# Optimization experiments

Measured on AMD Instinct MI355X. Metric: run time of the kernel, lower is better.

The kernel has to match this reference:

```python
import jax, jax.numpy as jnp
import numpy as np

H, K, D, HID, B = 8, 2048, 64, 1024, 8192
TEMP = 1.0
LN_EPS = 1e-5


def setup_inputs() -> dict:
    key = jax.random.key(0)
    ks = jax.random.split(key, 6)
    s = lambda k, shape, scale=0.02: jax.random.normal(k, shape, jnp.float32) * scale
    return dict(
        z=jax.random.normal(ks[0], (B, HID), jnp.float32),
        w1=s(ks[1], (H, HID, 2 * D)),
        b1=jnp.zeros((H, 2 * D), jnp.float32),
        w2=s(ks[2], (H, 2 * D, D)),
        b2=jnp.zeros((H, D), jnp.float32),
        ln_g=jnp.ones((H, D), jnp.float32),
        ln_b=jnp.zeros((H, D), jnp.float32),
        codebooks=jax.random.normal(ks[3], (H, K, D), jnp.float32) * 0.1,
        dec_w=s(ks[4], (H, D, HID // H)),
        dec_b=jnp.zeros((H, HID // H), jnp.float32),
    )


def reference(z, w1, b1, w2, b2, ln_g, ln_b, codebooks, dec_w, dec_b):
    sg = jax.lax.stop_gradient
    Bf = z.shape[0]
    # per-head projection MLP (all heads fused via einsum): [B,HID] -> [B,H,2D] -> [B,H,D]
    h1 = jax.nn.gelu(jnp.einsum('bi,hio->bho', z, w1) + b1, approximate=False)
    zh = jnp.einsum('bho,hod->bhd', h1, w2) + b2
    mu = zh.mean(-1, keepdims=True)
    var = zh.var(-1, keepdims=True)  # biased, as torch LayerNorm
    z_heads = (zh - mu) / jnp.sqrt(var + LN_EPS) * ln_g + ln_b  # [B,H,D]
    # squared-distance to codebooks: ||z||^2 + ||c||^2 - 2 z.c  -> [B,H,K]
    z_sq = (z_heads ** 2).sum(-1)[..., None]          # [B,H,1]
    c_sq = (codebooks ** 2).sum(-1)[None]             # [1,H,K]
    zc = jnp.einsum('bhd,hkd->bhk', z_heads, codebooks)
    dists = z_sq + c_sq - 2.0 * zc
    idx = jnp.argmin(dists, axis=-1)                  # [B,H] int
    z_q = codebooks[jnp.arange(H)[None, :], idx]      # gather -> [B,H,D]
    # per-head decoders then concat -> [B,HID]
    dec = lambda x: (jnp.einsum('bhd,hdo->bho', x, dec_w) + dec_b).reshape(Bf, -1)
    z_q_dec = dec(z_q)
    z_proj = dec(z_heads)
    z_q_st = z_proj + sg(z_q_dec - z_proj)
    commit = jnp.mean((z_proj - sg(z_q_dec)) ** 2)
    codebook_loss = jnp.mean((sg(z_proj) - z_q_dec) ** 2)
    # entropy regularizer over soft assignment probs
    probs = jax.nn.softmax(-dists * TEMP, axis=-1)    # [B,H,K]
    avg_probs = probs.mean(0)                         # [H,K]
    entropy = -(avg_probs * jnp.log(avg_probs + 1e-8)).sum(-1).mean()
    entropy_loss = 1.0 - entropy / np.float32(np.log(K))
    # orthogonality: pairwise co-occurrence deviation from independence
    p = jnp.zeros((H, K), jnp.float32).at[jnp.arange(H)[None, :], idx].add(1.0) / Bf  # [H,K]
    ortho = jnp.float32(0.0)
    cnt = 0
    for i in range(H):
        for j in range(i + 1, H):
            co = jnp.zeros((K, K), jnp.float32).at[idx[:, i], idx[:, j]].add(1.0) / (Bf + 1e-8)
            expected = p[i][:, None] * p[j][None, :]
            ortho = ortho + jnp.mean(jnp.abs(co - expected))
            cnt += 1
    ortho = ortho / cnt
    return z_q_st, idx, commit, codebook_loss, entropy_loss, ortho, sg(z_heads)
```

## Files before the change

kernel.cpp:

```cpp
#include <hip/hip_runtime.h>
#include <math.h>

#define H 8
#define KK 2048
#define DD 64
#define HIDN 1024
#define BB 8192
#define TWO_D 128
#define OO 128

#define WS_CSQ   1048576
#define WS_ZSQ   1064960
#define WS_IDX   1130496
#define WS_AVGP  1196032
#define WS_HIST  1212416
#define WS_ACC   1228800
#define WS_ZERO_BYTES ((16384 + 16384 + 4) * 4)

#define OUT_ZQ 0
#define OUT_IDX 8388608
#define OUT_COMMIT 8454144
#define OUT_CBL 8454145
#define OUT_ENT 8454146
#define OUT_ORTHO 8454147
#define OUT_ZH 8454148
#define W2P_OFF 3145728

typedef __attribute__((ext_vector_type(8))) short bf16x8;
typedef __attribute__((ext_vector_type(4))) float f32x4;

__device__ inline unsigned short bf16_rne(float x) {
    union { float f; unsigned u; } c; c.f = x;
    unsigned r = c.u + 0x7FFFu + ((c.u >> 16) & 1u);
    return (unsigned short)(r >> 16);
}
__device__ inline float bf16_f32(unsigned short h) {
    union { unsigned u; float f; } c; c.u = ((unsigned)h) << 16;
    return c.f;
}
__device__ inline void split3(float x, short* hh, short* mm, short* ll) {
    unsigned short h_ = bf16_rne(x);
    float r1 = x - bf16_f32(h_);
    unsigned short m_ = bf16_rne(r1);
    float r2 = r1 - bf16_f32(m_);
    unsigned short l_ = bf16_rne(r2);
    *hh = (short)h_; *mm = (short)m_; *ll = (short)l_;
}

__device__ inline void gload_lds16(const void* g, void* l) {
    __builtin_amdgcn_global_load_lds(
        (const __attribute__((address_space(1))) unsigned int*)g,
        (__attribute__((address_space(3))) unsigned int*)l, 16, 0, 0);
}

__global__ __launch_bounds__(256) void k_pre_w1(const float* __restrict__ w1, float* outp) {
    short* w1p = (short*)outp;
    int h = blockIdx.x >> 5, kc = blockIdx.x & 31;
    int t = threadIdx.x;
    int l = t & 63, w = t >> 6;
    int lb = l & 15, lg = l >> 4;
#pragma unroll
    for (int oi = 0; oi < 2; ++oi) {
        int ot = w + oi * 4;
        union { short e[8]; bf16x8 v; } uh, um, ul;
#pragma unroll
        for (int j = 0; j < 8; ++j) {
            float x = w1[(size_t)(h * HIDN + kc * 32 + lg * 8 + j) * TWO_D + ot * 16 + lb];
            split3(x, &uh.e[j], &um.e[j], &ul.e[j]);
        }
        size_t base = (((size_t)(h * 32 + kc) * 8 + ot) * 3) * 512 + l * 8;
        *(bf16x8*)(w1p + base) = uh.v;
        *(bf16x8*)(w1p + base + 512) = um.v;
        *(bf16x8*)(w1p + base + 1024) = ul.v;
    }
}

__global__ __launch_bounds__(256) void k_pre_w2(const float* __restrict__ w2, float* outp) {
    short* w2p = (short*)outp + W2P_OFF;
    int h = blockIdx.x;
    int t = threadIdx.x;
    int l = t & 63, w = t >> 6;
    int lb = l & 15, lg = l >> 4;
#pragma unroll
    for (int i = 0; i < 4; ++i) {
        int fr = w * 4 + i;
        int dt = fr >> 2, oc = fr & 3;
        union { short e[8]; bf16x8 v; } uh, um, ul;
#pragma unroll
        for (int j = 0; j < 8; ++j) {
            float x = w2[(size_t)(h * TWO_D + oc * 32 + lg * 8 + j) * DD + dt * 16 + lb];
            split3(x, &uh.e[j], &um.e[j], &ul.e[j]);
        }
        size_t base = (((size_t)(h * 4 + dt) * 4 + oc) * 3) * 512 + l * 8;
        *(bf16x8*)(w2p + base) = uh.v;
        *(bf16x8*)(w2p + base + 512) = um.v;
        *(bf16x8*)(w2p + base + 1024) = ul.v;
    }
}

__global__ __launch_bounds__(256) void k_pre(const float* __restrict__ cb, float* __restrict__ ws) {
    int h = blockIdx.x >> 3, kb = blockIdx.x & 7;
    int t = threadIdx.x;
    int lb = t & 15, lg = (t >> 4) & 3;
    short* stg = (short*)ws;
#pragma unroll
    for (int p = 0; p < 4; ++p) {
        int tloc = p * 4 + (t >> 6);
        int T = kb * 16 + tloc;
        int k = T * 16 + lb;
        const float* row = cb + (size_t)(h * KK + k) * DD;
        float4 a0 = *(const float4*)(row + lg * 8);
        float4 a1 = *(const float4*)(row + lg * 8 + 4);
        float4 c0 = *(const float4*)(row + 32 + lg * 8);
        float4 c1 = *(const float4*)(row + 32 + lg * 8 + 4);
        float v0[8] = {a0.x, a0.y, a0.z, a0.w, a1.x, a1.y, a1.z, a1.w};
        float v1[8] = {c0.x, c0.y, c0.z, c0.w, c1.x, c1.y, c1.z, c1.w};
        union { short e[8]; bf16x8 v; } h0, h1, l0, l1;
        float s = 0.f;
#pragma unroll
        for (int j = 0; j < 8; ++j) {
            float x = v0[j];
            s = fmaf(x, x, s);
            unsigned short hb = bf16_rne(x);
            h0.e[j] = (short)hb;
            l0.e[j] = (short)bf16_rne(x - bf16_f32(hb));
            float y = v1[j];
            s = fmaf(y, y, s);
            unsigned short hb2 = bf16_rne(y);
            h1.e[j] = (short)hb2;
            l1.e[j] = (short)bf16_rne(y - bf16_f32(hb2));
        }
        size_t base = (((size_t)(h * 128 + T) * 4) * 64 + (t & 63)) * 8;
        *(bf16x8*)(stg + base) = h0.v;
        *(bf16x8*)(stg + base + 512) = h1.v;
        *(bf16x8*)(stg + base + 1024) = l0.v;
        *(bf16x8*)(stg + base + 1536) = l1.v;
        s += __shfl_xor(s, 16);
        s += __shfl_xor(s, 32);
        if (lg == 0) ws[WS_CSQ + h * KK + k] = s;
    }
}

__global__ __launch_bounds__(512, 4) void k1(const float* __restrict__ z, const float* __restrict__ b1,
                                             const float* __restrict__ b2, const float* __restrict__ lng,
                                             const float* __restrict__ lnb, float* out,
                                             float* __restrict__ ws) {
    __shared__ char SM[51200];
    int t = threadIdx.x;
    int h = blockIdx.y;
    int b0 = blockIdx.x * 64;
    int w = t >> 6, l = t & 63;
    int rg = w >> 1, wc = w & 1;
    int lb = l & 15, lg = l >> 4;

    const short* w2p = (const short*)out + W2P_OFF;
    const char* w1h = (const char*)out + (size_t)h * (32 * 24576);
    const float* zrow = z + (size_t)(b0 + rg * 16 + lb) * HIDN + lg * 8;

    {
        char* lb0 = SM + (t >> 6) * 1024;
        const char* gb = w1h + t * 16;
#pragma unroll
        for (int r = 0; r < 3; ++r) gload_lds16(gb + r * 8192, lb0 + r * 8192);
#pragma unroll
        for (int r = 0; r < 3; ++r) gload_lds16(gb + 24576 + r * 8192, lb0 + 24576 + r * 8192);
    }
    float4 zA = *(const float4*)(zrow);
    float4 zB = *(const float4*)(zrow + 4);
    __syncthreads();

    f32x4 acc[4];
#pragma unroll
    for (int i = 0; i < 4; ++i) acc[i] = (f32x4){0.f, 0.f, 0.f, 0.f};

#pragma unroll
    for (int c = 0; c < 32; ++c) {
        if (c > 0) {
            if (c < 31) asm volatile("s_waitcnt vmcnt(3)" ::: "memory");
            else        asm volatile("s_waitcnt vmcnt(0)" ::: "memory");
            __builtin_amdgcn_sched_barrier(0);
            __builtin_amdgcn_s_barrier();
            __builtin_amdgcn_sched_barrier(0);
        }
        {
            float zc[8] = {zA.x, zA.y, zA.z, zA.w, zB.x, zB.y, zB.z, zB.w};
            union { short e[8]; bf16x8 v; } uh, um, ul;
#pragma unroll
            for (int j = 0; j < 8; ++j) split3(zc[j], &uh.e[j], &um.e[j], &ul.e[j]);
            bf16x8 bh = uh.v, bm = um.v, blo = ul.v;
            const char* bp = SM + (c & 1) * 24576;
#pragma unroll
            for (int ot = 0; ot < 4; ++ot) {
                const char* fb = bp + (wc * 4 + ot) * 3072 + l * 16;
                bf16x8 ah = *(const bf16x8*)(fb);
                bf16x8 am = *(const bf16x8*)(fb + 1024);
                bf16x8 al = *(const bf16x8*)(fb + 2048);
                f32x4 cc = acc[ot];
                cc = __builtin_amdgcn_mfma_f32_16x16x32_bf16(ah, bh, cc, 0, 0, 0);
                cc = __builtin_amdgcn_mfma_f32_16x16x32_bf16(ah, bm, cc, 0, 0, 0);
                cc = __builtin_amdgcn_mfma_f32_16x16x32_bf16(am, bh, cc, 0, 0, 0);
                cc = __builtin_amdgcn_mfma_f32_16x16x32_bf16(ah, blo, cc, 0, 0, 0);
                cc = __builtin_amdgcn_mfma_f32_16x16x32_bf16(al, bh, cc, 0, 0, 0);
                cc = __builtin_amdgcn_mfma_f32_16x16x32_bf16(am, bm, cc, 0, 0, 0);
                acc[ot] = cc;
            }
        }
        __builtin_amdgcn_sched_barrier(0);
        __builtin_amdgcn_s_barrier();
        __builtin_amdgcn_sched_barrier(0);
        if (c < 31) {
            zA = *(const float4*)(zrow + (c + 1) * 32);
            zB = *(const float4*)(zrow + (c + 1) * 32 + 4);
        }
        if (c + 2 < 32) {
            char* lb0 = SM + (c & 1) * 24576 + (t >> 6) * 1024;
            const char* gb = w1h + (size_t)(c + 2) * 24576 + t * 16;
#pragma unroll
            for (int r = 0; r < 3; ++r) gload_lds16(gb + r * 8192, lb0 + r * 8192);
        }
    }
    __syncthreads();

    float* h1L = (float*)SM;
    float* zhL = (float*)(SM + 33792);

#pragma unroll
    for (int ot = 0; ot < 4; ++ot)
#pragma unroll
        for (int r = 0; r < 4; ++r) {
            int o = (wc * 4 + ot) * 16 + lg * 4 + r;
            float x = acc[ot][r] + b1[h * TWO_D + o];
            float gl = 0.5f * x * (1.0f + erff(x * 0.70710678118654752f));
            h1L[(rg * 16 + lb) * 132 + o] = gl;
        }
    __syncthreads();

    f32x4 a2[2];
    a2[0] = (f32x4){0.f, 0.f, 0.f, 0.f};
    a2[1] = (f32x4){0.f, 0.f, 0.f, 0.f};
#pragma unroll
    for (int oc = 0; oc < 4; ++oc) {
        const float* hr = h1L + (rg * 16 + lb) * 132 + oc * 32 + lg * 8;
        union { short e[8]; bf16x8 v; } uh, um, ul;
#pragma unroll
        for (int j = 0; j < 8; ++j) split3(hr[j], &uh.e[j], &um.e[j], &ul.e[j]);
        bf16x8 bh = uh.v, bm = um.v, blo = ul.v;
#pragma unroll
        for (int dti = 0; dti < 2; ++dti) {
            int dt = wc * 2 + dti;
            const short* fb = w2p + (((size_t)(h * 4 + dt) * 4 + oc) * 3) * 512 + l * 8;
            bf16x8 ah = *(const bf16x8*)(fb);
            bf16x8 am = *(const bf16x8*)(fb + 512);
            bf16x8 al = *(const bf16x8*)(fb + 1024);
            f32x4 cc = a2[dti];
            cc = __builtin_amdgcn_mfma_f32_16x16x32_bf16(ah, bh, cc, 0, 0, 0);
            cc = __builtin_amdgcn_mfma_f32_16x16x32_bf16(ah, bm, cc, 0, 0, 0);
            cc = __builtin_amdgcn_mfma_f32_16x16x32_bf16(am, bh, cc, 0, 0, 0);
            cc = __builtin_amdgcn_mfma_f32_16x16x32_bf16(ah, blo, cc, 0, 0, 0);
            cc = __builtin_amdgcn_mfma_f32_16x16x32_bf16(al, bh, cc, 0, 0, 0);
            cc = __builtin_amdgcn_mfma_f32_16x16x32_bf16(am, bm, cc, 0, 0, 0);
            a2[dti] = cc;
        }
    }
#pragma unroll
    for (int dti = 0; dti < 2; ++dti)
#pragma unroll
        for (int r = 0; r < 4; ++r) {
            int d = (wc * 2 + dti) * 16 + lg * 4 + r;
            zhL[(rg * 16 + lb) * 68 + d] = a2[dti][r] + b2[h * DD + d];
        }
    __syncthreads();

    {
        int row = t >> 3, c0 = (t & 7) * 8;
        const float* zr = zhL + row * 68 + c0;
        float v[8];
#pragma unroll
        for (int j = 0; j < 8; ++j) v[j] = zr[j];
        float s = 0.f;
#pragma unroll
        for (int j = 0; j < 8; ++j) s += v[j];
        s += __shfl_xor(s, 1); s += __shfl_xor(s, 2); s += __shfl_xor(s, 4);
        float mu = s * (1.0f / 64.0f);
        float vv = 0.f;
#pragma unroll
        for (int j = 0; j < 8; ++j) { float d = v[j] - mu; vv = fmaf(d, d, vv); }
        vv += __shfl_xor(vv, 1); vv += __shfl_xor(vv, 2); vv += __shfl_xor(vv, 4);
        float rstd = 1.0f / sqrtf(vv * (1.0f / 64.0f) + 1e-5f);
        float zn[8]; float ss = 0.f;
#pragma unroll
        for (int j = 0; j < 8; ++j) {
            float x = (v[j] - mu) * rstd * lng[h * DD + c0 + j] + lnb[h * DD + c0 + j];
            zn[j] = x; ss = fmaf(x, x, ss);
        }
        ss += __shfl_xor(ss, 1); ss += __shfl_xor(ss, 2); ss += __shfl_xor(ss, 4);
        int brow = b0 + row;
        if ((t & 7) == 0) ws[WS_ZSQ + brow * H + h] = ss;
        float4 s0 = {zn[0], zn[1], zn[2], zn[3]};
        float4 s1 = {zn[4], zn[5], zn[6], zn[7]};
        *(float4*)(out + OUT_ZH + (size_t)(brow * H + h) * DD + c0) = s0;
        *(float4*)(out + OUT_ZH + (size_t)(brow * H + h) * DD + c0 + 4) = s1;
    }
}

#define MARGIN 0.05f
__device__ inline void stage32(const char* gsrc, short* lbuf, int t) {
    char* lb_ = (char*)lbuf + (t >> 6) * 1024;
    const char* gb = gsrc + t * 16;
    gload_lds16(gb, lb_);
    gload_lds16(gb + 16384, lb_ + 16384);
}
__global__ __launch_bounds__(1024, 4) void k2(const float* __restrict__ cb,
                                              float* __restrict__ out, float* __restrict__ ws) {
    __shared__ short bufs[3][16384];
    __shared__ float zt[32][68];
    __shared__ float redM[256], redS[256], redE[256];
    __shared__ int   redK[256];
    __shared__ float paccL[2048];

    int t = threadIdx.x;
    int h = blockIdx.y;
    int b0 = blockIdx.x * 32;
    int w = t >> 6, l = t & 63;
    int rg = w >> 3, kg = w & 7;
    int lb = l & 15, lg = l >> 4;
    int rmy = rg * 16 + lb;
    int myb = b0 + rmy;

    const char* stgbase = (const char*)ws + (size_t)h * 128 * 4096;

    stage32(stgbase, bufs[0], t);
    stage32(stgbase + 32768, bufs[1], t);
    stage32(stgbase + 65536, bufs[2], t);
    for (int i = t; i < 2048; i += 1024) paccL[i] = 0.f;
#pragma unroll
    for (int i = 0; i < 2; ++i) {
        int q = t + i * 1024;
        int r = q >> 6, d = q & 63;
        zt[r][d] = out[OUT_ZH + (size_t)((b0 + r) * H + h) * DD + d];
    }
    __syncthreads();

    float zsq = ws[WS_ZSQ + myb * H + h];

    bf16x8 bh[2], bl[2];
#pragma unroll
    for (int s = 0; s < 2; ++s) {
        const float* zr = &zt[rmy][s * 32 + lg * 8];
        union { short e[8]; bf16x8 v; } uh, ul;
#pragma unroll
        for (int j = 0; j < 8; ++j) {
            float x = zr[j];
            unsigned short hb = bf16_rne(x);
            uh.e[j] = (short)hb;
            ul.e[j] = (short)bf16_rne(x - bf16_f32(hb));
        }
        bh[s] = uh.v; bl[s] = ul.v;
    }

    f32x4 acc[16];
#pragma unroll
    for (int a = 0; a < 16; ++a) acc[a] = (f32x4){0.f, 0.f, 0.f, 0.f};

#pragma unroll
    for (int c = 0; c < 16; ++c) {
        if (c > 0) {
            if (c <= 13)      asm volatile("s_waitcnt vmcnt(4)" ::: "memory");
            else if (c == 14) asm volatile("s_waitcnt vmcnt(2)" ::: "memory");
            else              asm volatile("s_waitcnt vmcnt(0)" ::: "memory");
            __builtin_amdgcn_sched_barrier(0);
            __builtin_amdgcn_s_barrier();
            __builtin_amdgcn_sched_barrier(0);
        }
        {
            const short* fb = bufs[c % 3] + kg * 2048 + l * 8;
            bf16x8 A0 = *(const bf16x8*)(fb);
            bf16x8 A1 = *(const bf16x8*)(fb + 512);
            bf16x8 L0 = *(const bf16x8*)(fb + 1024);
            bf16x8 L1 = *(const bf16x8*)(fb + 1536);
            f32x4 cc = acc[c];
            cc = __builtin_amdgcn_mfma_f32_16x16x32_bf16(A0, bh[0], cc, 0, 0, 0);
            cc = __builtin_amdgcn_mfma_f32_16x16x32_bf16(A0, bl[0], cc, 0, 0, 0);
            cc = __builtin_amdgcn_mfma_f32_16x16x32_bf16(L0, bh[0], cc, 0, 0, 0);
            cc = __builtin_amdgcn_mfma_f32_16x16x32_bf16(A1, bh[1], cc, 0, 0, 0);
            cc = __builtin_amdgcn_mfma_f32_16x16x32_bf16(A1, bl[1], cc, 0, 0, 0);
            cc = __builtin_amdgcn_mfma_f32_16x16x32_bf16(L1, bh[1], cc, 0, 0, 0);
            acc[c] = cc;
        }
        if (c < 15) {
            __builtin_amdgcn_sched_barrier(0);
            __builtin_amdgcn_s_barrier();
            __builtin_amdgcn_sched_barrier(0);
            if (c + 3 < 16)
                stage32(stgbase + (size_t)(c + 3) * 32768, bufs[c % 3], t);
        }
    }

    float Mloc = 3.4e38f;
#pragma unroll
    for (int ai = 0; ai < 16; ++ai) {
        int k0 = (8 * ai + kg) * 16;
        float4 cs = *(const float4*)(ws + WS_CSQ + h * KK + k0 + lg * 4);
        f32x4 a = acc[ai];
        float d0 = (zsq + cs.x) - 2.f * a[0];
        float d1 = (zsq + cs.y) - 2.f * a[1];
        float d2 = (zsq + cs.z) - 2.f * a[2];
        float d3 = (zsq + cs.w) - 2.f * a[3];
        acc[ai] = (f32x4){d0, d1, d2, d3};
        Mloc = fminf(Mloc, fminf(fminf(d0, d1), fminf(d2, d3)));
    }
    Mloc = fminf(Mloc, __shfl_xor(Mloc, 16));
    Mloc = fminf(Mloc, __shfl_xor(Mloc, 32));
    if (l < 16) redM[rg * 128 + kg * 16 + lb] = Mloc;
    __syncthreads();
    float Mb = redM[rg * 128 + lb];
#pragma unroll
    for (int g = 1; g < 8; ++g) Mb = fminf(Mb, redM[rg * 128 + g * 16 + lb]);

    float T = Mb + MARGIN;
    float Sloc = 0.f;
    unsigned long long mask = 0ull;
#pragma unroll
    for (int ai = 0; ai < 16; ++ai) {
        f32x4 d = acc[ai];
        f32x4 e;
#pragma unroll
        for (int r = 0; r < 4; ++r) {
            float dv = d[r];
            if (dv <= T) mask |= 1ull << (ai * 4 + r);
            float ev = __expf(Mb - dv);
            Sloc += ev;
            e[r] = ev;
        }
        acc[ai] = e;
    }

    float eBest = 3.4e38f; int kBest = 0x7FFFFFFF;
    {
        const float* zr0 = &zt[rmy][0];
        unsigned long long m = mask;
        while (m) {
            int i = (int)__ffsll(m) - 1;
            m &= m - 1;
            int ai = i >> 2, r = i & 3;
            int k = (8 * ai + kg) * 16 + lg * 4 + r;
            const float4* crow = (const float4*)(cb + (size_t)(h * KK + k) * DD);
            float s = 0.f;
#pragma unroll 1
            for (int q = 0; q < 16; ++q) {
                float4 cv = crow[q];
                s = fmaf(zr0[q * 4 + 0], cv.x, s);
                s = fmaf(zr0[q * 4 + 1], cv.y, s);
                s = fmaf(zr0[q * 4 + 2], cv.z, s);
                s = fmaf(zr0[q * 4 + 3], cv.w, s);
            }
            float ex = (zsq + ws[WS_CSQ + h * KK + k]) - 2.f * s;
            if (ex < eBest || (ex == eBest && k < kBest)) { eBest = ex; kBest = k; }
        }
    }
#pragma unroll
    for (int off = 16; off <= 32; off <<= 1) {
        Sloc += __shfl_xor(Sloc, off);
        float oe = __shfl_xor(eBest, off);
        int ok = __shfl_xor(kBest, off);
        if (oe < eBest || (oe == eBest && ok < kBest)) { eBest = oe; kBest = ok; }
    }
    if (l < 16) {
        redS[rg * 128 + kg * 16 + lb] = Sloc;
        redE[rg * 128 + kg * 16 + lb] = eBest;
        redK[rg * 128 + kg * 16 + lb] = kBest;
    }
    __syncthreads();
    float Sb = redS[rg * 128 + lb];
#pragma unroll
    for (int g = 1; g < 8; ++g) Sb += redS[rg * 128 + g * 16 + lb];

    if (kg == 0 && l < 16) {
        float eB = redE[rg * 128 + lb]; int kB = redK[rg * 128 + lb];
#pragma unroll
        for (int g = 1; g < 8; ++g) {
            float oe = redE[rg * 128 + g * 16 + lb];
            int ok = redK[rg * 128 + g * 16 + lb];
            if (oe < eB || (oe == eB && ok < kB)) { eB = oe; kB = ok; }
        }
        out[OUT_IDX + myb * H + h] = (float)kB;
        ((int*)ws)[WS_IDX + myb * H + h] = kB;
        atomicAdd(((unsigned*)ws) + WS_HIST + h * KK + kB, 1u);
    }

    float invS = 1.0f / Sb;
#pragma unroll
    for (int ai = 0; ai < 16; ++ai) {
        f32x4 e = acc[ai];
        float p0 = e[0] * invS;
        float p1 = e[1] * invS;
        float p2 = e[2] * invS;
        float p3 = e[3] * invS;
#pragma unroll
        for (int off = 1; off < 16; off <<= 1) {
            p0 += __shfl_xor(p0, off);
            p1 += __shfl_xor(p1, off);
            p2 += __shfl_xor(p2, off);
            p3 += __shfl_xor(p3, off);
        }
        if (lb == 0) {
            int k0 = (8 * ai + kg) * 16 + lg * 4;
            atomicAdd(&paccL[k0 + 0], p0);
            atomicAdd(&paccL[k0 + 1], p1);
            atomicAdd(&paccL[k0 + 2], p2);
            atomicAdd(&paccL[k0 + 3], p3);
        }
    }
    __syncthreads();
    for (int i = t; i < 2048; i += 1024)
        atomicAdd(ws + WS_AVGP + h * KK + i, paccL[i]);
}

__global__ __launch_bounds__(256, 2) void k3(const float* __restrict__ cb, const float* __restrict__ dw,
                                             const float* __restrict__ db, float* __restrict__ out,
                                             float* __restrict__ ws) {
    __shared__ float zqt[32][65];
    __shared__ float zht[32][65];
    __shared__ float dwt[64][128];
    __shared__ int idxs[32];
    __shared__ double redc[4];
    int t = threadIdx.x;
    int h = blockIdx.y;
    int b0 = blockIdx.x * 32;
    if (t < 32) idxs[t] = ((const int*)ws)[WS_IDX + (b0 + t) * H + h];
    __syncthreads();
#pragma unroll
    for (int p = 0; p < 8; ++p) {
        int q = t + 256 * p;
        int r = q >> 6, d = q & 63;
        zqt[r][d] = cb[(size_t)(h * KK + idxs[r]) * DD + d];
        zht[r][d] = out[OUT_ZH + (size_t)((b0 + r) * H + h) * DD + d];
    }
#pragma unroll
    for (int p = 0; p < 8; ++p) {
        int q = t + 256 * p;
        int r = q >> 5, c4 = q & 31;
        *(float4*)(&dwt[r][c4 * 4]) = *(const float4*)(dw + (size_t)(h * DD + r) * OO + c4 * 4);
    }
    __syncthreads();
    int rg = t >> 4, cg = t & 15;
    float aq[2][8], ap[2][8];
#pragma unroll
    for (int i = 0; i < 2; ++i)
#pragma unroll
        for (int j = 0; j < 8; ++j) { aq[i][j] = 0.f; ap[i][j] = 0.f; }
#pragma unroll 4
    for (int d = 0; d < 64; ++d) {
        float q0 = zqt[rg * 2][d], q1 = zqt[rg * 2 + 1][d];
        float p0 = zht[rg * 2][d], p1 = zht[rg * 2 + 1][d];
        float4 wa = *(const float4*)(&dwt[d][cg * 8]);
        float4 wb = *(const float4*)(&dwt[d][cg * 8 + 4]);
        float ww[8] = {wa.x, wa.y, wa.z, wa.w, wb.x, wb.y, wb.z, wb.w};
#pragma unroll
        for (int j = 0; j < 8; ++j) {
            aq[0][j] = fmaf(q0, ww[j], aq[0][j]);
            aq[1][j] = fmaf(q1, ww[j], aq[1][j]);
            ap[0][j] = fmaf(p0, ww[j], ap[0][j]);
            ap[1][j] = fmaf(p1, ww[j], ap[1][j]);
        }
    }
    float lsum = 0.f;
#pragma unroll
    for (int i = 0; i < 2; ++i) {
        float vq4[8];
#pragma unroll
        for (int j = 0; j < 8; ++j) {
            float bb = db[h * OO + cg * 8 + j];
            float vq = aq[i][j] + bb;
            float vp = ap[i][j] + bb;
            vq4[j] = vp + (vq - vp);
            float e = vp - vq;
            lsum = fmaf(e, e, lsum);
        }
        float4 s0 = {vq4[0], vq4[1], vq4[2], vq4[3]};
        float4 s1 = {vq4[4], vq4[5], vq4[6], vq4[7]};
        size_t o = (size_t)(b0 + rg * 2 + i) * HIDN + h * OO + cg * 8;
        *(float4*)(out + OUT_ZQ + o) = s0;
        *(float4*)(out + OUT_ZQ + o + 4) = s1;
    }
#pragma unroll
    for (int off = 1; off < 64; off <<= 1) lsum += __shfl_xor(lsum, off);
    if ((t & 63) == 0) redc[t >> 6] = (double)lsum;
    __syncthreads();
    if (t == 0) atomicAdd((double*)(ws + WS_ACC), redc[0] + redc[1] + redc[2] + redc[3]);
}

__global__ __launch_bounds__(256) void k6(float* __restrict__ ws) {
    __shared__ unsigned slots[16384];
    __shared__ unsigned cnts[16384];
    int t = threadIdx.x;
    int bid = blockIdx.x;
    int pi = 0, pj = 1;
    {
        int c = 0;
        for (int a = 0; a < H; ++a)
            for (int b = a + 1; b < H; ++b) { if (c == bid) { pi = a; pj = b; } ++c; }
    }
    for (int s = t; s < 16384; s += 256) { slots[s] = 0xFFFFFFFFu; cnts[s] = 0u; }
    __syncthreads();
    const int* idxi = ((const int*)ws) + WS_IDX;
    for (int b = t; b < BB; b += 256) {
        unsigned key = ((unsigned)idxi[b * H + pi] << 11) | (unsigned)idxi[b * H + pj];
        unsigned p = (key * 2654435761u) >> 18;
        while (true) {
            unsigned old = atomicCAS(&slots[p], 0xFFFFFFFFu, key);
            if (old == 0xFFFFFFFFu || old == key) { atomicAdd(&cnts[p], 1u); break; }
            p = (p + 1) & 16383u;
        }
    }
    __syncthreads();
    const unsigned* hist = ((const unsigned*)ws) + WS_HIST;
    double loc = 0.0;
    for (int s = t; s < 16384; s += 256) {
        unsigned key = slots[s];
        if (key != 0xFFFFFFFFu) {
            int ki = (int)(key >> 11), kj = (int)(key & 2047u);
            float c = (float)cnts[s] * (1.0f / 8192.0f);
            float piv = (float)hist[pi * KK + ki] * (1.0f / 8192.0f);
            float pjv = (float)hist[pj * KK + kj] * (1.0f / 8192.0f);
            float e = piv * pjv;
            loc += (double)fabsf(c - e) - (double)e;
        }
    }
    double spi = 0.0, spj = 0.0;
    for (int k = t; k < KK; k += 256) {
        spi += (double)hist[pi * KK + k];
        spj += (double)hist[pj * KK + k];
    }
#pragma unroll
    for (int off = 1; off < 64; off <<= 1) {
        loc += __shfl_xor(loc, off);
        spi += __shfl_xor(spi, off);
        spj += __shfl_xor(spj, off);
    }
    __syncthreads();
    double* sc = (double*)cnts;
    if ((t & 63) == 0) { int w = t >> 6; sc[w] = loc; sc[4 + w] = spi; sc[8 + w] = spj; }
    __syncthreads();
    if (t == 0) {
        double L = sc[0] + sc[1] + sc[2] + sc[3];
        double SPI = (sc[4] + sc[5] + sc[6] + sc[7]) / 8192.0;
        double SPJ = (sc[8] + sc[9] + sc[10] + sc[11]) / 8192.0;
        atomicAdd(((double*)(ws + WS_ACC)) + 1, L + SPI * SPJ);
    }
}

__global__ __launch_bounds__(256) void k4(float* __restrict__ out, float* __restrict__ ws) {
    __shared__ double red[256];
    int t = threadIdx.x;
    double tot = 0.0;
    for (int h = 0; h < H; ++h) {
        double s = 0.0;
        for (int k = t; k < KK; k += 256) {
            double a = (double)ws[WS_AVGP + h * KK + k] / 8192.0;
            s += a * log(a + 1e-8);
        }
        tot += s;
    }
    red[t] = tot;
    __syncthreads();
    for (int off = 128; off; off >>= 1) {
        if (t < off) red[t] += red[t + off];
        __syncthreads();
    }
    if (t == 0) {
        double entropy = -red[0] / 8.0;
        out[OUT_ENT] = (float)(1.0 - entropy / log(2048.0));
        double ca = *(const double*)(ws + WS_ACC);
        float cm = (float)(ca / (8192.0 * 1024.0));
        out[OUT_COMMIT] = cm;
        out[OUT_CBL] = cm;
        double oa = *(((const double*)(ws + WS_ACC)) + 1);
        out[OUT_ORTHO] = (float)(oa / (28.0 * 4194304.0));
    }
}

extern "C" void kernel_launch(void* const* d_in, const int* in_sizes, int n_in,
                              void* d_out, int out_size, void* d_ws, size_t ws_size,
                              hipStream_t stream) {
    (void)in_sizes; (void)n_in; (void)out_size; (void)ws_size;
    const float* z   = (const float*)d_in[0];
    const float* w1  = (const float*)d_in[1];
    const float* b1  = (const float*)d_in[2];
    const float* w2  = (const float*)d_in[3];
    const float* b2  = (const float*)d_in[4];
    const float* lng = (const float*)d_in[5];
    const float* lnb = (const float*)d_in[6];
    const float* cb  = (const float*)d_in[7];
    const float* dw  = (const float*)d_in[8];
    const float* db  = (const float*)d_in[9];
    float* out = (float*)d_out;
    float* ws = (float*)d_ws;

    hipMemsetAsync(ws + WS_AVGP, 0, WS_ZERO_BYTES, stream);
    k_pre_w1<<<256, 256, 0, stream>>>(w1, out);
    k_pre_w2<<<8, 256, 0, stream>>>(w2, out);
    k_pre<<<64, 256, 0, stream>>>(cb, ws);
    k1<<<dim3(128, 8), 512, 0, stream>>>(z, b1, b2, lng, lnb, out, ws);
    k2<<<dim3(256, 8), 1024, 0, stream>>>(cb, out, ws);
    k3<<<dim3(256, 8), 256, 0, stream>>>(cb, dw, db, out, ws);
    k6<<<28, 256, 0, stream>>>(ws);
    k4<<<1, 256, 0, stream>>>(out, ws);
}
```

Baseline: 547.3 us.

## Drop codebook low-bf16 split and transpose MFMA operands in distance kernel

The codebook is now staged as a single bf16 term instead of a hi/lo pair. This halves the staged bytes and the LDS buffers, and cuts the MFMA count per chunk from six to four. The MFMA operands are swapped so each lane holds one codebook column and four batch rows, which turns the softmax-sum and probability reductions into cheaper in-lane accumulation. c_sq and z_sq are also cached in LDS. The argmin candidate margin is widened to make up for the lower codebook precision, at the risk of more fp32 rescoring work and possible near-tie misses.

```diff
diff --git a/kernel.cpp b/kernel.cpp
--- a/kernel.cpp
+++ b/kernel.cpp
@@ -101,12 +101,12 @@
 __global__ __launch_bounds__(256) void k_pre(const float* __restrict__ cb, float* __restrict__ ws) {
     int h = blockIdx.x >> 3, kb = blockIdx.x & 7;
     int t = threadIdx.x;
-    int lb = t & 15, lg = (t >> 4) & 3;
+    int l = t & 63;
+    int lb = l & 15, lg = l >> 4;
     short* stg = (short*)ws;
 #pragma unroll
     for (int p = 0; p < 4; ++p) {
-        int tloc = p * 4 + (t >> 6);
-        int T = kb * 16 + tloc;
+        int T = kb * 16 + p * 4 + (t >> 6);
         int k = T * 16 + lb;
         const float* row = cb + (size_t)(h * KK + k) * DD;
         float4 a0 = *(const float4*)(row + lg * 8);
@@ -115,26 +115,20 @@
         float4 c1 = *(const float4*)(row + 32 + lg * 8 + 4);
         float v0[8] = {a0.x, a0.y, a0.z, a0.w, a1.x, a1.y, a1.z, a1.w};
         float v1[8] = {c0.x, c0.y, c0.z, c0.w, c1.x, c1.y, c1.z, c1.w};
-        union { short e[8]; bf16x8 v; } h0, h1, l0, l1;
+        union { short e[8]; bf16x8 v; } h0, h1;
         float s = 0.f;
 #pragma unroll
         for (int j = 0; j < 8; ++j) {
             float x = v0[j];
             s = fmaf(x, x, s);
-            unsigned short hb = bf16_rne(x);
-            h0.e[j] = (short)hb;
-            l0.e[j] = (short)bf16_rne(x - bf16_f32(hb));
+            h0.e[j] = (short)bf16_rne(x);
             float y = v1[j];
             s = fmaf(y, y, s);
-            unsigned short hb2 = bf16_rne(y);
-            h1.e[j] = (short)hb2;
-            l1.e[j] = (short)bf16_rne(y - bf16_f32(hb2));
-        }
-        size_t base = (((size_t)(h * 128 + T) * 4) * 64 + (t & 63)) * 8;
+            h1.e[j] = (short)bf16_rne(y);
+        }
+        size_t base = ((size_t)(h * 128 + T)) * 1024 + l * 8;
         *(bf16x8*)(stg + base) = h0.v;
         *(bf16x8*)(stg + base + 512) = h1.v;
-        *(bf16x8*)(stg + base + 1024) = l0.v;
-        *(bf16x8*)(stg + base + 1536) = l1.v;
         s += __shfl_xor(s, 16);
         s += __shfl_xor(s, 32);
         if (lg == 0) ws[WS_CSQ + h * KK + k] = s;
@@ -303,19 +297,20 @@
     }
 }
 
-#define MARGIN 0.05f
-__device__ inline void stage32(const char* gsrc, short* lbuf, int t) {
+#define MARGIN 0.10f
+__device__ inline void stage16(const char* gsrc, short* lbuf, int t) {
     char* lb_ = (char*)lbuf + (t >> 6) * 1024;
-    const char* gb = gsrc + t * 16;
-    gload_lds16(gb, lb_);
-    gload_lds16(gb + 16384, lb_ + 16384);
+    gload_lds16(gsrc + t * 16, lb_);
 }
 __global__ __launch_bounds__(1024, 4) void k2(const float* __restrict__ cb,
                                               float* __restrict__ out, float* __restrict__ ws) {
-    __shared__ short bufs[3][16384];
+    __shared__ short bufs[3][8192];
     __shared__ float zt[32][68];
-    __shared__ float redM[256], redS[256], redE[256];
-    __shared__ int   redK[256];
+    __shared__ float csqL[2048];
+    __shared__ float zsqL[32];
+    __shared__ float redM[8][32], redS[8][32], redE[8][32];
+    __shared__ int   redK[8][32];
+    __shared__ float MbL[32], SbL[32];
     __shared__ float paccL[2048];
 
     int t = threadIdx.x;
@@ -325,23 +320,24 @@
     int rg = w >> 3, kg = w & 7;
     int lb = l & 15, lg = l >> 4;
     int rmy = rg * 16 + lb;
-    int myb = b0 + rmy;
-
-    const char* stgbase = (const char*)ws + (size_t)h * 128 * 4096;
-
-    stage32(stgbase, bufs[0], t);
-    stage32(stgbase + 32768, bufs[1], t);
-    stage32(stgbase + 65536, bufs[2], t);
-    for (int i = t; i < 2048; i += 1024) paccL[i] = 0.f;
+
+    const char* stgbase = (const char*)ws + (size_t)h * 262144;
+
+    stage16(stgbase, bufs[0], t);
+    stage16(stgbase + 16384, bufs[1], t);
+    stage16(stgbase + 32768, bufs[2], t);
+    for (int i = t; i < 2048; i += 1024) {
+        paccL[i] = 0.f;
+        csqL[i] = ws[WS_CSQ + h * KK + i];
+    }
 #pragma unroll
     for (int i = 0; i < 2; ++i) {
         int q = t + i * 1024;
         int r = q >> 6, d = q & 63;
         zt[r][d] = out[OUT_ZH + (size_t)((b0 + r) * H + h) * DD + d];
     }
-    __syncthreads();
-
-    float zsq = ws[WS_ZSQ + myb * H + h];
+    if (t < 32) zsqL[t] = ws[WS_ZSQ + (b0 + t) * H + h];
+    __syncthreads();
 
     bf16x8 bh[2], bl[2];
 #pragma unroll
@@ -365,26 +361,22 @@
 #pragma unroll
     for (int c = 0; c < 16; ++c) {
         if (c > 0) {
-            if (c <= 13)      asm volatile("s_waitcnt vmcnt(4)" ::: "memory");
-            else if (c == 14) asm volatile("s_waitcnt vmcnt(2)" ::: "memory");
+            if (c <= 13)      asm volatile("s_waitcnt vmcnt(2)" ::: "memory");
+            else if (c == 14) asm volatile("s_waitcnt vmcnt(1)" ::: "memory");
             else              asm volatile("s_waitcnt vmcnt(0)" ::: "memory");
             __builtin_amdgcn_sched_barrier(0);
             __builtin_amdgcn_s_barrier();
             __builtin_amdgcn_sched_barrier(0);
         }
         {
-            const short* fb = bufs[c % 3] + kg * 2048 + l * 8;
-            bf16x8 A0 = *(const bf16x8*)(fb);
-            bf16x8 A1 = *(const bf16x8*)(fb + 512);
-            bf16x8 L0 = *(const bf16x8*)(fb + 1024);
-            bf16x8 L1 = *(const bf16x8*)(fb + 1536);
+            const short* fb = bufs[c % 3] + kg * 1024 + l * 8;
+            bf16x8 C0 = *(const bf16x8*)(fb);
+            bf16x8 C1 = *(const bf16x8*)(fb + 512);
             f32x4 cc = acc[c];
-            cc = __builtin_amdgcn_mfma_f32_16x16x32_bf16(A0, bh[0], cc, 0, 0, 0);
-            cc = __builtin_amdgcn_mfma_f32_16x16x32_bf16(A0, bl[0], cc, 0, 0, 0);
-            cc = __builtin_amdgcn_mfma_f32_16x16x32_bf16(L0, bh[0], cc, 0, 0, 0);
-            cc = __builtin_amdgcn_mfma_f32_16x16x32_bf16(A1, bh[1], cc, 0, 0, 0);
-            cc = __builtin_amdgcn_mfma_f32_16x16x32_bf16(A1, bl[1], cc, 0, 0, 0);
-            cc = __builtin_amdgcn_mfma_f32_16x16x32_bf16(L1, bh[1], cc, 0, 0, 0);
+            cc = __builtin_amdgcn_mfma_f32_16x16x32_bf16(bh[0], C0, cc, 0, 0, 0);
+            cc = __builtin_amdgcn_mfma_f32_16x16x32_bf16(bl[0], C0, cc, 0, 0, 0);
+            cc = __builtin_amdgcn_mfma_f32_16x16x32_bf16(bh[1], C1, cc, 0, 0, 0);
+            cc = __builtin_amdgcn_mfma_f32_16x16x32_bf16(bl[1], C1, cc, 0, 0, 0);
             acc[c] = cc;
         }
         if (c < 15) {
@@ -392,34 +384,48 @@
             __builtin_amdgcn_s_barrier();
             __builtin_amdgcn_sched_barrier(0);
             if (c + 3 < 16)
-                stage32(stgbase + (size_t)(c + 3) * 32768, bufs[c % 3], t);
-        }
-    }
-
-    float Mloc = 3.4e38f;
+                stage16(stgbase + (size_t)(c + 3) * 16384, bufs[c % 3], t);
+        }
+    }
+
+    float zsqv[4];
+#pragma unroll
+    for (int r = 0; r < 4; ++r) zsqv[r] = zsqL[rg * 16 + lg * 4 + r];
+    float mn[4] = {3.4e38f, 3.4e38f, 3.4e38f, 3.4e38f};
 #pragma unroll
     for (int ai = 0; ai < 16; ++ai) {
-        int k0 = (8 * ai + kg) * 16;
-        float4 cs = *(const float4*)(ws + WS_CSQ + h * KK + k0 + lg * 4);
+        float cs = csqL[(8 * ai + kg) * 16 + lb];
         f32x4 a = acc[ai];
-        float d0 = (zsq + cs.x) - 2.f * a[0];
-        float d1 = (zsq + cs.y) - 2.f * a[1];
-        float d2 = (zsq + cs.z) - 2.f * a[2];
-        float d3 = (zsq + cs.w) - 2.f * a[3];
-        acc[ai] = (f32x4){d0, d1, d2, d3};
-        Mloc = fminf(Mloc, fminf(fminf(d0, d1), fminf(d2, d3)));
-    }
-    Mloc = fminf(Mloc, __shfl_xor(Mloc, 16));
-    Mloc = fminf(Mloc, __shfl_xor(Mloc, 32));
-    if (l < 16) redM[rg * 128 + kg * 16 + lb] = Mloc;
-    __syncthreads();
-    float Mb = redM[rg * 128 + lb];
-#pragma unroll
-    for (int g = 1; g < 8; ++g) Mb = fminf(Mb, redM[rg * 128 + g * 16 + lb]);
-
-    float T = Mb + MARGIN;
-    float Sloc = 0.f;
-    unsigned long long mask = 0ull;
+        f32x4 d;
+#pragma unroll
+        for (int r = 0; r < 4; ++r) {
+            float dv = (zsqv[r] + cs) - 2.f * a[r];
+            d[r] = dv;
+            mn[r] = fminf(mn[r], dv);
+        }
+        acc[ai] = d;
+    }
+#pragma unroll
+    for (int off = 1; off < 16; off <<= 1)
+#pragma unroll
+        for (int r = 0; r < 4; ++r) mn[r] = fminf(mn[r], __shfl_xor(mn[r], off));
+    if (lb == 0)
+#pragma unroll
+        for (int r = 0; r < 4; ++r) redM[kg][rg * 16 + lg * 4 + r] = mn[r];
+    __syncthreads();
+    if (t < 32) {
+        float m = redM[0][t];
+#pragma unroll
+        for (int g = 1; g < 8; ++g) m = fminf(m, redM[g][t]);
+        MbL[t] = m;
+    }
+    __syncthreads();
+    float Mb[4];
+#pragma unroll
+    for (int r = 0; r < 4; ++r) Mb[r] = MbL[rg * 16 + lg * 4 + r];
+
+    float S[4] = {0.f, 0.f, 0.f, 0.f};
+    unsigned mk0 = 0, mk1 = 0, mk2 = 0, mk3 = 0;
 #pragma unroll
     for (int ai = 0; ai < 16; ++ai) {
         f32x4 d = acc[ai];
@@ -427,23 +433,36 @@
 #pragma unroll
         for (int r = 0; r < 4; ++r) {
             float dv = d[r];
-            if (dv <= T) mask |= 1ull << (ai * 4 + r);
-            float ev = __expf(Mb - dv);
-            Sloc += ev;
+            float ev = __expf(Mb[r] - dv);
+            S[r] += ev;
             e[r] = ev;
+            bool cand = dv <= Mb[r] + MARGIN;
+            if (r == 0) mk0 |= cand ? (1u << ai) : 0u;
+            if (r == 1) mk1 |= cand ? (1u << ai) : 0u;
+            if (r == 2) mk2 |= cand ? (1u << ai) : 0u;
+            if (r == 3) mk3 |= cand ? (1u << ai) : 0u;
         }
         acc[ai] = e;
     }
-
-    float eBest = 3.4e38f; int kBest = 0x7FFFFFFF;
-    {
-        const float* zr0 = &zt[rmy][0];
-        unsigned long long m = mask;
+#pragma unroll
+    for (int off = 1; off < 16; off <<= 1)
+#pragma unroll
+        for (int r = 0; r < 4; ++r) S[r] += __shfl_xor(S[r], off);
+    if (lb == 0)
+#pragma unroll
+        for (int r = 0; r < 4; ++r) redS[kg][rg * 16 + lg * 4 + r] = S[r];
+
+    float eB[4] = {3.4e38f, 3.4e38f, 3.4e38f, 3.4e38f};
+    int kB[4] = {0x7FFFFFFF, 0x7FFFFFFF, 0x7FFFFFFF, 0x7FFFFFFF};
+#pragma unroll
+    for (int r = 0; r < 4; ++r) {
+        unsigned m = (r == 0) ? mk0 : (r == 1) ? mk1 : (r == 2) ? mk2 : mk3;
+        const float* zr0 = &zt[rg * 16 + lg * 4 + r][0];
+        float eBest = 3.4e38f; int kBest = 0x7FFFFFFF;
         while (m) {
-            int i = (int)__ffsll(m) - 1;
+            int ai = (int)__ffs(m) - 1;
             m &= m - 1;
-            int ai = i >> 2, r = i & 3;
-            int k = (8 * ai + kg) * 16 + lg * 4 + r;
+            int k = (8 * ai + kg) * 16 + lb;
             const float4* crow = (const float4*)(cb + (size_t)(h * KK + k) * DD);
             float s = 0.f;
 #pragma unroll 1
@@ -454,62 +473,56 @@
                 s = fmaf(zr0[q * 4 + 2], cv.z, s);
                 s = fmaf(zr0[q * 4 + 3], cv.w, s);
             }
-            float ex = (zsq + ws[WS_CSQ + h * KK + k]) - 2.f * s;
+            float ex = (zsqv[r] + csqL[k]) - 2.f * s;
             if (ex < eBest || (ex == eBest && k < kBest)) { eBest = ex; kBest = k; }
         }
-    }
-#pragma unroll
-    for (int off = 16; off <= 32; off <<= 1) {
-        Sloc += __shfl_xor(Sloc, off);
-        float oe = __shfl_xor(eBest, off);
-        int ok = __shfl_xor(kBest, off);
-        if (oe < eBest || (oe == eBest && ok < kBest)) { eBest = oe; kBest = ok; }
-    }
-    if (l < 16) {
-        redS[rg * 128 + kg * 16 + lb] = Sloc;
-        redE[rg * 128 + kg * 16 + lb] = eBest;
-        redK[rg * 128 + kg * 16 + lb] = kBest;
-    }
-    __syncthreads();
-    float Sb = redS[rg * 128 + lb];
-#pragma unroll
-    for (int g = 1; g < 8; ++g) Sb += redS[rg * 128 + g * 16 + lb];
-
-    if (kg == 0 && l < 16) {
-        float eB = redE[rg * 128 + lb]; int kB = redK[rg * 128 + lb];
+        eB[r] = eBest; kB[r] = kBest;
+    }
+#pragma unroll
+    for (int off = 1; off < 16; off <<= 1)
+#pragma unroll
+        for (int r = 0; r < 4; ++r) {
+            float oe = __shfl_xor(eB[r], off);
+            int ok = __shfl_xor(kB[r], off);
+            if (oe < eB[r] || (oe == eB[r] && ok < kB[r])) { eB[r] = oe; kB[r] = ok; }
+        }
+    if (lb == 0)
+#pragma unroll
+        for (int r = 0; r < 4; ++r) {
+            redE[kg][rg * 16 + lg * 4 + r] = eB[r];
+            redK[kg][rg * 16 + lg * 4 + r] = kB[r];
+        }
+    __syncthreads();
+    if (t < 32) {
+        float Sv = redS[0][t];
+#pragma unroll
+        for (int g = 1; g < 8; ++g) Sv += redS[g][t];
+        SbL[t] = Sv;
+        float e0 = redE[0][t]; int k0_ = redK[0][t];
 #pragma unroll
         for (int g = 1; g < 8; ++g) {
-            float oe = redE[rg * 128 + g * 16 + lb];
-            int ok = redK[rg * 128 + g * 16 + lb];
-            if (oe < eB || (oe == eB && ok < kB)) { eB = oe; kB = ok; }
-        }
-        out[OUT_IDX + myb * H + h] = (float)kB;
-        ((int*)ws)[WS_IDX + myb * H + h] = kB;
-        atomicAdd(((unsigned*)ws) + WS_HIST + h * KK + kB, 1u);
-    }
-
-    float invS = 1.0f / Sb;
+            float oe = redE[g][t]; int ok = redK[g][t];
+            if (oe < e0 || (oe == e0 && ok < k0_)) { e0 = oe; k0_ = ok; }
+        }
+        out[OUT_IDX + (b0 + t) * H + h] = (float)k0_;
+        ((int*)ws)[WS_IDX + (b0 + t) * H + h] = k0_;
+        atomicAdd(((unsigned*)ws) + WS_HIST + h * KK + k0_, 1u);
+    }
+    __syncthreads();
+    float invS[4];
+#pragma unroll
+    for (int r = 0; r < 4; ++r) invS[r] = 1.0f / SbL[rg * 16 + lg * 4 + r];
+
 #pragma unroll
     for (int ai = 0; ai < 16; ++ai) {
         f32x4 e = acc[ai];
-        float p0 = e[0] * invS;
-        float p1 = e[1] * invS;
-        float p2 = e[2] * invS;
-        float p3 = e[3] * invS;
-#pragma unroll
-        for (int off = 1; off < 16; off <<= 1) {
-            p0 += __shfl_xor(p0, off);
-            p1 += __shfl_xor(p1, off);
-            p2 += __shfl_xor(p2, off);
-            p3 += __shfl_xor(p3, off);
-        }
-        if (lb == 0) {
-            int k0 = (8 * ai + kg) * 16 + lg * 4;
-            atomicAdd(&paccL[k0 + 0], p0);
-            atomicAdd(&paccL[k0 + 1], p1);
-            atomicAdd(&paccL[k0 + 2], p2);
-            atomicAdd(&paccL[k0 + 3], p3);
-        }
+        float v = e[0] * invS[0];
+        v = fmaf(e[1], invS[1], v);
+        v = fmaf(e[2], invS[2], v);
+        v = fmaf(e[3], invS[3], v);
+        v += __shfl_xor(v, 16);
+        v += __shfl_xor(v, 32);
+        if (lg == 0) atomicAdd(&paccL[(8 * ai + kg) * 16 + lb], v);
     }
     __syncthreads();
     for (int i = t; i < 2048; i += 1024)
```

New measurement: 537.4 us. No clear change (-1.8%).
